# Kernel tuning notes

Measured on AMD Instinct MI355X. Metric: run time of the kernel, lower is better.

Reference implementation:

```python
import jax, jax.numpy as jnp
import numpy as np

N = 65536      # number of nodes being updated
EMBED = 1024   # embed_size
G = 256        # g_size (per-head dim)
MLP = 256      # mlp_size
H = 4          # n_head


def setup_inputs() -> dict:
    key = jax.random.key(0)
    ks = jax.random.split(key, 8)
    s_in = 1.0 / np.sqrt(EMBED)
    s_g = 1.0 / np.sqrt(G)
    s_m = 1.0 / np.sqrt(MLP)
    s_hg = 1.0 / np.sqrt(H * G)
    return {
        "q": jax.random.normal(ks[0], (N, EMBED), jnp.float32),
        "rep": jax.random.normal(ks[1], (N, EMBED), jnp.float32),
        "Wq": jax.random.normal(ks[2], (EMBED, H * G), jnp.float32) * s_in,
        "Wk": jax.random.normal(ks[3], (EMBED, H * G), jnp.float32) * s_in,
        "Wv": jax.random.normal(ks[4], (EMBED, H * G), jnp.float32) * s_in,
        "W1": jax.random.normal(ks[5], (H, G, MLP), jnp.float32) * s_g,
        "b1": jnp.zeros((H, MLP), jnp.float32),
        "W2": jax.random.normal(ks[6], (H, MLP, G), jnp.float32) * s_m,
        "b2": jnp.zeros((H, G), jnp.float32),
        "Ws": jax.random.normal(ks[7], (H * G, EMBED), jnp.float32) * s_hg,
    }


def reference(q, rep, Wq, Wk, Wv, W1, b1, W2, b2, Ws):
    # Per-head Q/K/V projections: [N, E] -> [N, H, G]
    n = q.shape[0]
    Qh = (q @ Wq).reshape(n, H, G)
    Kh = (rep @ Wk).reshape(n, H, G)
    Vh = (rep @ Wv).reshape(n, H, G)
    # Elementwise scaled attention gate (Q, K are per-node vectors -> 2D attn)
    gate = jax.nn.sigmoid(Qh * Kh * (1.0 / np.sqrt(G)))
    z = gate * Vh  # [N, H, G]
    # Per-head MLP (num_mlp = 1 block): G -> MLP -> G with ReLU
    h1 = jax.nn.relu(jnp.einsum('nhg,hgm->nhm', z, W1) + b1)
    z2 = jnp.einsum('nhm,hmg->nhg', h1, W2) + b2
    update_gate = z2.reshape(n, H * G)
    # update_attn_scale (no bias) + fused residual: h = Q - K + proj(gate)
    h = q - rep + update_gate @ Ws
    return h
```

## Files before the change

kernel.cpp:

```cpp
#include <hip/hip_runtime.h>
#include <hip/hip_bf16.h>


typedef __attribute__((ext_vector_type(8))) short bf16x8;
typedef __attribute__((ext_vector_type(4))) float f32x4;
typedef __attribute__((ext_vector_type(4))) short short4v;

#define AS1 __attribute__((address_space(1)))
#define AS3 __attribute__((address_space(3)))

static __device__ __forceinline__ short f2b(float x) {
  __hip_bfloat16 h = __float2bfloat16(x);
  return __builtin_bit_cast(short, h);
}
static __device__ __forceinline__ float b2f(short s) {
  unsigned u = ((unsigned)(unsigned short)s) << 16;
  return __builtin_bit_cast(float, u);
}

__global__ void cvt_bf16_2(const float* __restrict__ q, const float* __restrict__ rep,
                           short* __restrict__ qb, short* __restrict__ rb, long n) {
  const float* __restrict__ in = blockIdx.z ? rep : q;
  short* __restrict__ out = blockIdx.z ? rb : qb;
  long i = ((long)blockIdx.x * blockDim.x + threadIdx.x) * 4;
  const long stride = (long)gridDim.x * blockDim.x * 4;
  for (; i < n; i += stride) {
    float4 v = *(const float4*)(in + i);
    short4v o = { f2b(v.x), f2b(v.y), f2b(v.z), f2b(v.w) };
    *(short4v*)(out + i) = o;
  }
}

__global__ void prep_weights(
    const float* __restrict__ Wq, const float* __restrict__ Wk, const float* __restrict__ Wv,
    const float* __restrict__ W1, const float* __restrict__ W2, const float* __restrict__ Ws,
    short* __restrict__ wqt, short* __restrict__ wkt, short* __restrict__ wvt,
    short* __restrict__ w1t, short* __restrict__ w2t, short* __restrict__ wst)
{
  const int job = blockIdx.z;
  const float* src; short* dst; int R, C;
  if (job < 3)       { src = (job==0)?Wq:((job==1)?Wk:Wv); dst = (job==0)?wqt:((job==1)?wkt:wvt); R = 1024; C = 1024; }
  else if (job == 3) { src = Ws; dst = wst; R = 1024; C = 1024; }
  else if (job < 8)  { int h = job-4; src = W1 + h*65536; dst = w1t + h*65536; R = 256; C = 256; }
  else               { int h = job-8; src = W2 + h*65536; dst = w2t + h*65536; R = 256; C = 256; }
  const int c0 = blockIdx.x * 32, r0 = blockIdx.y * 32;
  if (c0 >= C || r0 >= R) return;
  __shared__ float t[32][33];
  for (int i = threadIdx.y; i < 32; i += 8)
    t[i][threadIdx.x] = src[(long)(r0 + i) * C + c0 + threadIdx.x];
  __syncthreads();
  for (int i = threadIdx.y; i < 32; i += 8)
    dst[(long)(c0 + i) * R + r0 + threadIdx.x] = f2b(t[threadIdx.x][i]);
}

template <int KDIM, int LDA, int LDB, bool RELU, bool BIAS, bool RESID, bool SWZ>
__global__ __launch_bounds__(512, 2) void gemm_bf16(
    const short* __restrict__ A, long zsa,
    const short* __restrict__ Bt, long zsb,
    void* __restrict__ outv, long ldc, long zsc,
    const float* __restrict__ bias, long zsbias,
    const short* __restrict__ qres, const short* __restrict__ rres)
{
  __shared__ __align__(16) short lA[4 * 8192];
  __shared__ __align__(16) short lB[4 * 8192];
  const int lane = threadIdx.x & 63, wave = threadIdx.x >> 6;
  const int wm = wave >> 2, wn = wave & 3;
  int bx = blockIdx.x, by = blockIdx.y;
  if (SWZ) {
    const int nbx = gridDim.x;
    const int flat = by * nbx + bx;
    const int chunk = (int)(gridDim.x * gridDim.y) >> 3;
    const int fid = (flat & 7) * chunk + (flat >> 3);
    bx = fid % nbx; by = fid / nbx;
  }
  const long bm = (long)by * 256;
  const int  bn = bx * 256;
  const int  zi = blockIdx.z;

  const short* Ab = A + (long)zi * zsa + bm * LDA;
  const short* Bb = Bt + (long)zi * zsb + (long)bn * LDB;
  constexpr int NS = KDIM / 32;
  const int g0 = lane >> 4;
  const int arow = wm * 128 + (lane & 15);
  const int bcol = wn * 64 + (lane & 15);

  const char* aP = (const char*)lA + arow * 64 + (((g0 ^ (arow >> 1)) & 3) << 4);
  const char* bP = (const char*)lB + bcol * 64 + (((g0 ^ (bcol >> 1)) & 3) << 4);

  const int rw = lane >> 2;
  const int gg = (lane & 3) ^ ((rw >> 1) & 3);
  const short* Asrc = Ab + (wave * 16 + rw) * LDA + (gg << 3);
  const short* Bsrc = Bb + (wave * 16 + rw) * LDB + (gg << 3);
  short* lAd = lA + wave * 16 * 32;
  short* lBd = lB + wave * 16 * 32;

  auto stA = [&](int slot, int s) {
    const int sc = s < NS ? s : NS - 1;
    const short* src = Asrc + sc * 32;
    short* d = lAd + slot * 8192;
    __builtin_amdgcn_global_load_lds((const AS1 void*)src,              (AS3 void*)d,        16, 0, 0);
    __builtin_amdgcn_global_load_lds((const AS1 void*)(src + 128*LDA),  (AS3 void*)(d+4096), 16, 0, 0);
  };
  auto stB = [&](int slot, int s) {
    const int sc = s < NS ? s : NS - 1;
    const short* src = Bsrc + sc * 32;
    short* d = lBd + slot * 8192;
    __builtin_amdgcn_global_load_lds((const AS1 void*)src,              (AS3 void*)d,        16, 0, 0);
    __builtin_amdgcn_global_load_lds((const AS1 void*)(src + 128*LDB),  (AS3 void*)(d+4096), 16, 0, 0);
  };

  stA(0, 0); stB(0, 0);
  stA(1, 1); stB(1, 1);
  stA(2, 2); stB(2, 2);
  asm volatile("s_waitcnt vmcnt(8)" ::: "memory");
  __builtin_amdgcn_s_barrier();

  f32x4 acc[8][4] = {};
  bf16x8 b[4];

#define PHASE(SLOT, MH, LOADB, STAGE_STMT, DOVM)                            \
  {                                                                         \
    if (LOADB) {                                                            \
      _Pragma("unroll")                                                     \
      for (int j = 0; j < 4; ++j)                                           \
        b[j] = *(const bf16x8*)(bP + (SLOT) * 16384 + j * 1024);            \
    }                                                                       \
    bf16x8 a[4];                                                            \
    _Pragma("unroll")                                                       \
    for (int i2 = 0; i2 < 4; ++i2)                                          \
      a[i2] = *(const bf16x8*)(aP + (SLOT) * 16384 + (MH) * 4096 + i2 * 1024); \
    STAGE_STMT;                                                             \
    if (DOVM) asm volatile("s_waitcnt vmcnt(8)" ::: "memory");              \
    asm volatile("" ::: "memory");                                          \
    __builtin_amdgcn_s_barrier();                                           \
    __builtin_amdgcn_s_setprio(1);                                          \
    _Pragma("unroll")                                                       \
    for (int i2 = 0; i2 < 4; ++i2)                                          \
      _Pragma("unroll")                                                     \
      for (int j = 0; j < 4; ++j)                                           \
        acc[(MH) * 4 + i2][j] = __builtin_amdgcn_mfma_f32_16x16x32_bf16(    \
            a[i2], b[j], acc[(MH) * 4 + i2][j], 0, 0, 0);                   \
    __builtin_amdgcn_s_setprio(0);                                          \
    asm volatile("" ::: "memory");                                          \
    __builtin_amdgcn_s_barrier();                                           \
  }

  for (int s = 0; s < NS; s += 4) {
    PHASE(0, 0, true,  stA(3, s + 3), false) PHASE(0, 1, false, stB(3, s + 3), true)
    PHASE(1, 0, true,  stA(0, s + 4), false) PHASE(1, 1, false, stB(0, s + 4), true)
    PHASE(2, 0, true,  stA(1, s + 5), false) PHASE(2, 1, false, stB(1, s + 5), true)
    PHASE(3, 0, true,  stA(2, s + 6), false) PHASE(3, 1, false, stB(2, s + 6), true)
  }
#undef PHASE

  #pragma unroll
  for (int i = 0; i < 8; ++i)
    #pragma unroll
    for (int j = 0; j < 4; ++j)
      #pragma unroll
      for (int r = 0; r < 4; ++r) {
        const int rl = wm * 128 + i * 16 + ((lane >> 4) << 2) + r;
        const int cl = wn * 64 + j * 16 + (lane & 15);
        float v = acc[i][j][r];
        if (BIAS) v += bias[(long)zi * zsbias + bn + cl];
        if (RELU) v = v > 0.0f ? v : 0.0f;
        const long row = bm + rl;
        const long gi = (long)zi * zsc + row * ldc + bn + cl;
        if (RESID) {
          ((float*)outv)[gi] = b2f(qres[gi]) - b2f(rres[gi]) + v;
        } else {
          ((short*)outv)[gi] = f2b(v);
        }
      }
}

__global__ __launch_bounds__(512, 2) void gemm_g23(
    const short* __restrict__ rb, const short* __restrict__ wkt,
    const short* __restrict__ wvt, const short* __restrict__ gh,
    short* __restrict__ zb)
{
  __shared__ __align__(16) short lA[4 * 8192];
  __shared__ __align__(16) short lK[4 * 4096];
  __shared__ __align__(16) short lV[4 * 4096];
  const int lane = threadIdx.x & 63, wave = threadIdx.x >> 6;
  const int wm = wave >> 2, wn = wave & 3;
  int bx = blockIdx.x, by = blockIdx.y;
  {
    const int flat = by * 8 + bx;
    const int chunk = (int)(gridDim.x * gridDim.y) >> 3;
    const int fid = (flat & 7) * chunk + (flat >> 3);
    bx = fid & 7; by = fid >> 3;
  }
  const long bm = (long)by * 256;
  const int  bn = bx * 128;

  const short* Ab = rb + bm * 1024;
  const short* Kb = wkt + (long)bn * 1024;
  const short* Vb = wvt + (long)bn * 1024;
  constexpr int NS = 32;
  const int g0 = lane >> 4;
  const int arow = wm * 128 + (lane & 15);
  const int bcol = wn * 32 + (lane & 15);

  const char* aP = (const char*)lA + arow * 64 + (((g0 ^ (arow >> 1)) & 3) << 4);
  const char* kP = (const char*)lK + bcol * 64 + (((g0 ^ (bcol >> 1)) & 3) << 4);
  const char* vP = (const char*)lV + bcol * 64 + (((g0 ^ (bcol >> 1)) & 3) << 4);

  const int rw = lane >> 2;
  const int gg = (lane & 3) ^ ((rw >> 1) & 3);
  const short* Asrc = Ab + (wave * 16 + rw) * 1024 + (gg << 3);
  const short* Ksrc = Kb + (wave * 16 + rw) * 1024 + (gg << 3);
  const short* Vsrc = Vb + (wave * 16 + rw) * 1024 + (gg << 3);
  short* lAd = lA + wave * 16 * 32;
  short* lKd = lK + wave * 16 * 32;
  short* lVd = lV + wave * 16 * 32;

  auto stA = [&](int slot, int s) {
    const int sc = s < NS ? s : NS - 1;
    const short* src = Asrc + sc * 32;
    short* d = lAd + slot * 8192;
    __builtin_amdgcn_global_load_lds((const AS1 void*)src,               (AS3 void*)d,        16, 0, 0);
    __builtin_amdgcn_global_load_lds((const AS1 void*)(src + 128*1024),  (AS3 void*)(d+4096), 16, 0, 0);
  };
  auto stKV = [&](int slot, int s) {
    const int sc = s < NS ? s : NS - 1;
    __builtin_amdgcn_global_load_lds((const AS1 void*)(Ksrc + sc * 32), (AS3 void*)(lKd + slot * 4096), 16, 0, 0);
    __builtin_amdgcn_global_load_lds((const AS1 void*)(Vsrc + sc * 32), (AS3 void*)(lVd + slot * 4096), 16, 0, 0);
  };

  stA(0, 0); stKV(0, 0);
  stA(1, 1); stKV(1, 1);
  stA(2, 2); stKV(2, 2);
  asm volatile("s_waitcnt vmcnt(8)" ::: "memory");
  __builtin_amdgcn_s_barrier();

  f32x4 ack[8][2] = {};
  f32x4 acv[8][2] = {};
  bf16x8 bk[2], bv[2];

#define PHASEG(SLOT, MH, LOADB, STAGE_STMT, DOVM)                           \
  {                                                                         \
    if (LOADB) {                                                            \
      _Pragma("unroll")                                                     \
      for (int j = 0; j < 2; ++j) {                                         \
        bk[j] = *(const bf16x8*)(kP + (SLOT) * 8192 + j * 1024);            \
        bv[j] = *(const bf16x8*)(vP + (SLOT) * 8192 + j * 1024);            \
      }                                                                     \
    }                                                                       \
    bf16x8 a[4];                                                            \
    _Pragma("unroll")                                                       \
    for (int i2 = 0; i2 < 4; ++i2)                                          \
      a[i2] = *(const bf16x8*)(aP + (SLOT) * 16384 + (MH) * 4096 + i2 * 1024); \
    STAGE_STMT;                                                             \
    if (DOVM) asm volatile("s_waitcnt vmcnt(8)" ::: "memory");              \
    asm volatile("" ::: "memory");                                          \
    __builtin_amdgcn_s_barrier();                                           \
    __builtin_amdgcn_s_setprio(1);                                          \
    _Pragma("unroll")                                                       \
    for (int i2 = 0; i2 < 4; ++i2)                                          \
      _Pragma("unroll")                                                     \
      for (int j = 0; j < 2; ++j) {                                         \
        ack[(MH) * 4 + i2][j] = __builtin_amdgcn_mfma_f32_16x16x32_bf16(    \
            a[i2], bk[j], ack[(MH) * 4 + i2][j], 0, 0, 0);                  \
        acv[(MH) * 4 + i2][j] = __builtin_amdgcn_mfma_f32_16x16x32_bf16(    \
            a[i2], bv[j], acv[(MH) * 4 + i2][j], 0, 0, 0);                  \
      }                                                                     \
    __builtin_amdgcn_s_setprio(0);                                          \
    asm volatile("" ::: "memory");                                          \
    __builtin_amdgcn_s_barrier();                                           \
  }

  for (int s = 0; s < NS; s += 4) {
    PHASEG(0, 0, true,  stA(3, s + 3), false) PHASEG(0, 1, false, stKV(3, s + 3), true)
    PHASEG(1, 0, true,  stA(0, s + 4), false) PHASEG(1, 1, false, stKV(0, s + 4), true)
    PHASEG(2, 0, true,  stA(1, s + 5), false) PHASEG(2, 1, false, stKV(1, s + 5), true)
    PHASEG(3, 0, true,  stA(2, s + 6), false) PHASEG(3, 1, false, stKV(2, s + 6), true)
  }
#undef PHASEG

  #pragma unroll
  for (int i = 0; i < 8; ++i)
    #pragma unroll
    for (int j = 0; j < 2; ++j)
      #pragma unroll
      for (int r = 0; r < 4; ++r) {
        const int rl = wm * 128 + i * 16 + ((lane >> 4) << 2) + r;
        const int cl = wn * 32 + j * 16 + (lane & 15);
        const long gi = (bm + rl) * 1024 + bn + cl;
        const float x = b2f(gh[gi]) * ack[i][j][r] * 0.0625f;
        const float gate = 1.0f / (1.0f + __expf(-x));
        zb[gi] = f2b(gate * acv[i][j][r]);
      }
}

__global__ __launch_bounds__(512) void gemm_mlp(
    const short* __restrict__ zb, const short* __restrict__ w1t,
    const short* __restrict__ w2t, const float* __restrict__ b1,
    const float* __restrict__ b2, short* __restrict__ ug)
{
  __shared__ __align__(16) char smem[163840];
  short* lA = (short*)smem;
  short* lB = (short*)(smem + 65536);
  short* stash = (short*)smem;
  short* w2b = (short*)(smem + 131072);

  const int lane = threadIdx.x & 63, wave = threadIdx.x >> 6;
  const int wm = wave >> 2, wn = wave & 3;
  const long bm = (long)blockIdx.y * 256;
  const int head = blockIdx.z;

  const int g0 = lane >> 4;
  const int arow = wm * 128 + (lane & 15);
  const int bcol = wn * 64 + (lane & 15);
  const int rw = lane >> 2;
  const int gg = (lane & 3) ^ ((rw >> 1) & 3);

  {
    const short* Ab = zb + bm * 1024 + head * 256;
    const short* Bb = w1t + head * 65536;
    const char* aP = (const char*)lA + arow * 64 + (((g0 ^ (arow >> 1)) & 3) << 4);
    const char* bP = (const char*)lB + bcol * 64 + (((g0 ^ (bcol >> 1)) & 3) << 4);
    const short* Asrc = Ab + (wave * 16 + rw) * 1024 + (gg << 3);
    const short* Bsrc = Bb + (wave * 16 + rw) * 256 + (gg << 3);
    short* lAd = lA + wave * 16 * 32;
    short* lBd = lB + wave * 16 * 32;

    auto stA = [&](int slot, int s) {
      const int sc = s < 8 ? s : 7;
      const short* src = Asrc + sc * 32;
      short* d = lAd + slot * 8192;
      __builtin_amdgcn_global_load_lds((const AS1 void*)src,              (AS3 void*)d,        16, 0, 0);
      __builtin_amdgcn_global_load_lds((const AS1 void*)(src + 128*1024), (AS3 void*)(d+4096), 16, 0, 0);
    };
    auto stB = [&](int slot, int s) {
      const int sc = s < 8 ? s : 7;
      const short* src = Bsrc + sc * 32;
      short* d = lBd + slot * 8192;
      __builtin_amdgcn_global_load_lds((const AS1 void*)src,              (AS3 void*)d,        16, 0, 0);
      __builtin_amdgcn_global_load_lds((const AS1 void*)(src + 128*256),  (AS3 void*)(d+4096), 16, 0, 0);
    };

    stA(0, 0); stB(0, 0);
    stA(1, 1); stB(1, 1);
    stA(2, 2); stB(2, 2);
    asm volatile("s_waitcnt vmcnt(8)" ::: "memory");
    __builtin_amdgcn_s_barrier();

    f32x4 acc[8][4] = {};
    bf16x8 b[4];

#define PHASE1(SLOT, MH, LOADB, STAGE_STMT, DOVM)                           \
    {                                                                       \
      if (LOADB) {                                                          \
        _Pragma("unroll")                                                   \
        for (int j = 0; j < 4; ++j)                                         \
          b[j] = *(const bf16x8*)(bP + (SLOT) * 16384 + j * 1024);          \
      }                                                                     \
      bf16x8 a[4];                                                          \
      _Pragma("unroll")                                                     \
      for (int i2 = 0; i2 < 4; ++i2)                                        \
        a[i2] = *(const bf16x8*)(aP + (SLOT) * 16384 + (MH) * 4096 + i2 * 1024); \
      STAGE_STMT;                                                           \
      if (DOVM) asm volatile("s_waitcnt vmcnt(8)" ::: "memory");            \
      asm volatile("" ::: "memory");                                        \
      __builtin_amdgcn_s_barrier();                                         \
      __builtin_amdgcn_s_setprio(1);                                        \
      _Pragma("unroll")                                                     \
      for (int i2 = 0; i2 < 4; ++i2)                                        \
        _Pragma("unroll")                                                   \
        for (int j = 0; j < 4; ++j)                                         \
          acc[(MH) * 4 + i2][j] = __builtin_amdgcn_mfma_f32_16x16x32_bf16(  \
              a[i2], b[j], acc[(MH) * 4 + i2][j], 0, 0, 0);                 \
      __builtin_amdgcn_s_setprio(0);                                        \
      asm volatile("" ::: "memory");                                        \
      __builtin_amdgcn_s_barrier();                                         \
    }

    for (int s = 0; s < 8; s += 4) {
      PHASE1(0, 0, true,  stA(3, s + 3), false) PHASE1(0, 1, false, stB(3, s + 3), true)
      PHASE1(1, 0, true,  stA(0, s + 4), false) PHASE1(1, 1, false, stB(0, s + 4), true)
      PHASE1(2, 0, true,  stA(1, s + 5), false) PHASE1(2, 1, false, stB(1, s + 5), true)
      PHASE1(3, 0, true,  stA(2, s + 6), false) PHASE1(3, 1, false, stB(2, s + 6), true)
    }
#undef PHASE1

    __syncthreads();
    #pragma unroll
    for (int i = 0; i < 8; ++i)
      #pragma unroll
      for (int j = 0; j < 4; ++j)
        #pragma unroll
        for (int r = 0; r < 4; ++r) {
          const int rl = wm * 128 + i * 16 + ((lane >> 4) << 2) + r;
          const int cl = wn * 64 + j * 16 + (lane & 15);
          float v = acc[i][j][r] + b1[head * 256 + cl];
          v = v > 0.0f ? v : 0.0f;
          stash[rl * 256 + ((((cl >> 3) ^ rl) & 31) << 3) + (cl & 7)] = f2b(v);
        }
    __syncthreads();
  }

  {
    const short* Wb = w2t + head * 65536;
    const short* Bsrc2 = Wb + (wave * 16 + rw) * 256 + (gg << 3);
    short* lBd2 = w2b + wave * 16 * 32;
    const char* b2P = (const char*)w2b + bcol * 64 + (((g0 ^ (bcol >> 1)) & 3) << 4);

    auto stW = [&](int slot, int s) {
      const int sc = s < 8 ? s : 7;
      const short* src = Bsrc2 + sc * 32;
      short* d = lBd2 + slot * 8192;
      __builtin_amdgcn_global_load_lds((const AS1 void*)src,             (AS3 void*)d,        16, 0, 0);
      __builtin_amdgcn_global_load_lds((const AS1 void*)(src + 128*256), (AS3 void*)(d+4096), 16, 0, 0);
    };

    stW(0, 0);
    asm volatile("s_waitcnt vmcnt(0)" ::: "memory");
    __builtin_amdgcn_s_barrier();

    f32x4 acc2[8][4] = {};
    bf16x8 br[4];

    for (int s = 0; s < 8; ++s) {
      const int sl = s & 1;
      const int ks = s * 4 + g0;

#define PHASE2(MH, LOADB, STAGE_STMT, DOVM)                                 \
      {                                                                     \
        if (LOADB) {                                                        \
          _Pragma("unroll")                                                 \
          for (int j = 0; j < 4; ++j)                                       \
            br[j] = *(const bf16x8*)(b2P + sl * 16384 + j * 1024);          \
        }                                                                   \
        bf16x8 a[4];                                                        \
        _Pragma("unroll")                                                   \
        for (int i2 = 0; i2 < 4; ++i2) {                                    \
          const int row = arow + (MH) * 64 + i2 * 16;                       \
          a[i2] = *(const bf16x8*)(stash + row * 256 + (((ks ^ row) & 31) << 3)); \
        }                                                                   \
        STAGE_STMT;                                                         \
        if (DOVM) asm volatile("s_waitcnt vmcnt(0)" ::: "memory");          \
        asm volatile("" ::: "memory");                                      \
        __builtin_amdgcn_s_barrier();                                       \
        __builtin_amdgcn_s_setprio(1);                                      \
        _Pragma("unroll")                                                   \
        for (int i2 = 0; i2 < 4; ++i2)                                      \
          _Pragma("unroll")                                                 \
          for (int j = 0; j < 4; ++j)                                       \
            acc2[(MH) * 4 + i2][j] = __builtin_amdgcn_mfma_f32_16x16x32_bf16( \
                a[i2], br[j], acc2[(MH) * 4 + i2][j], 0, 0, 0);             \
        __builtin_amdgcn_s_setprio(0);                                      \
        asm volatile("" ::: "memory");                                      \
        __builtin_amdgcn_s_barrier();                                       \
      }

      PHASE2(0, true,  stW(sl ^ 1, s + 1), false)
      PHASE2(1, false, {}, true)
#undef PHASE2
    }

    #pragma unroll
    for (int i = 0; i < 8; ++i)
      #pragma unroll
      for (int j = 0; j < 4; ++j)
        #pragma unroll
        for (int r = 0; r < 4; ++r) {
          const int rl = wm * 128 + i * 16 + ((lane >> 4) << 2) + r;
          const int cl = wn * 64 + j * 16 + (lane & 15);
          const float v = acc2[i][j][r] + b2[head * 256 + cl];
          ug[(bm + rl) * 1024 + head * 256 + cl] = f2b(v);
        }
  }
}

extern "C" void kernel_launch(void* const* d_in, const int* in_sizes, int n_in,
                              void* d_out, int out_size, void* d_ws, size_t ws_size,
                              hipStream_t stream) {
  const float* q   = (const float*)d_in[0];
  const float* rep = (const float*)d_in[1];
  const float* Wq  = (const float*)d_in[2];
  const float* Wk  = (const float*)d_in[3];
  const float* Wv  = (const float*)d_in[4];
  const float* W1  = (const float*)d_in[5];
  const float* b1  = (const float*)d_in[6];
  const float* W2  = (const float*)d_in[7];
  const float* b2  = (const float*)d_in[8];
  const float* Ws  = (const float*)d_in[9];
  float* out = (float*)d_out;

  const long NE = 67108864L;
  char* ws = (char*)d_ws;
  short* qb  = (short*)(ws);
  short* rb  = (short*)(ws + NE * 2);
  short* gh  = (short*)(ws + NE * 4);
  short* zb  = (short*)(ws + NE * 6);
  short* ugb = gh;
  char*  wp  = ws + NE * 8;
  short* wqt = (short*)(wp);
  short* wkt = (short*)(wp + 2097152);
  short* wvt = (short*)(wp + 4194304);
  short* wst = (short*)(wp + 6291456);
  short* w1t = (short*)(wp + 8388608);
  short* w2t = (short*)(wp + 8912896);

  cvt_bf16_2<<<dim3(2048, 1, 2), 256, 0, stream>>>(q, rep, qb, rb, NE);
  prep_weights<<<dim3(32, 32, 12), dim3(32, 8), 0, stream>>>(
      Wq, Wk, Wv, W1, W2, Ws, wqt, wkt, wvt, w1t, w2t, wst);

  gemm_bf16<1024, 1024, 1024, false, false, false, true><<<dim3(4, 256), 512, 0, stream>>>(
      qb, 0, wqt, 0, gh, 1024, 0, nullptr, 0, nullptr, nullptr);
  gemm_g23<<<dim3(8, 256), 512, 0, stream>>>(rb, wkt, wvt, gh, zb);
  gemm_mlp<<<dim3(1, 256, 4), 512, 0, stream>>>(zb, w1t, w2t, b1, b2, ugb);
  gemm_bf16<1024, 1024, 1024, false, false, true, true><<<dim3(4, 256), 512, 0, stream>>>(
      ugb, 0, wst, 0, out, 1024, 0, nullptr, 0, qb, rb);
}
```

Before: 1.002 ms.

## Fuse Q projection into gated K/V GEMM kernel, dropping Q intermediate

The separate Q-projection GEMM and its bf16 intermediate buffer are removed. Q is now computed in the same kernel as K and V, so the sigmoid gate uses the Q accumulator directly instead of reading a stored Q tile. To fit the extra operand tiles in LDS, the pipeline is cut from four stages to two, and each stage waits for all outstanding loads (vmcnt(0)). This saves one kernel launch plus the write and reread of a 128MB intermediate. In exchange it adds accumulator register pressure and gives less latency hiding.

```diff
diff --git a/kernel.cpp b/kernel.cpp
--- a/kernel.cpp
+++ b/kernel.cpp
@@ -174,14 +174,19 @@
       }
 }
 
-__global__ __launch_bounds__(512, 2) void gemm_g23(
-    const short* __restrict__ rb, const short* __restrict__ wkt,
-    const short* __restrict__ wvt, const short* __restrict__ gh,
+__global__ __launch_bounds__(512, 2) void gemm_g123(
+    const short* __restrict__ qb,
+    const short* __restrict__ rb,
+    const short* __restrict__ wqt,
+    const short* __restrict__ wkt,
+    const short* __restrict__ wvt,
     short* __restrict__ zb)
 {
-  __shared__ __align__(16) short lA[4 * 8192];
-  __shared__ __align__(16) short lK[4 * 4096];
-  __shared__ __align__(16) short lV[4 * 4096];
+  __shared__ __align__(16) short lAq[2 * 8192];
+  __shared__ __align__(16) short lAr[2 * 8192];
+  __shared__ __align__(16) short lQ[2 * 4096];
+  __shared__ __align__(16) short lK[2 * 4096];
+  __shared__ __align__(16) short lV[2 * 4096];
   const int lane = threadIdx.x & 63, wave = threadIdx.x >> 6;
   const int wm = wave >> 2, wn = wave & 3;
   int bx = blockIdx.x, by = blockIdx.y;
@@ -194,7 +199,9 @@
   const long bm = (long)by * 256;
   const int  bn = bx * 128;
 
-  const short* Ab = rb + bm * 1024;
+  const short* Aqb = qb + bm * 1024;
+  const short* Arb = rb + bm * 1024;
+  const short* Qb = wqt + (long)bn * 1024;
   const short* Kb = wkt + (long)bn * 1024;
   const short* Vb = wvt + (long)bn * 1024;
   constexpr int NS = 32;
@@ -202,81 +209,95 @@
   const int arow = wm * 128 + (lane & 15);
   const int bcol = wn * 32 + (lane & 15);
 
-  const char* aP = (const char*)lA + arow * 64 + (((g0 ^ (arow >> 1)) & 3) << 4);
+  const char* aPq = (const char*)lAq + arow * 64 + (((g0 ^ (arow >> 1)) & 3) << 4);
+  const char* aPr = (const char*)lAr + arow * 64 + (((g0 ^ (arow >> 1)) & 3) << 4);
+  const char* qP = (const char*)lQ + bcol * 64 + (((g0 ^ (bcol >> 1)) & 3) << 4);
   const char* kP = (const char*)lK + bcol * 64 + (((g0 ^ (bcol >> 1)) & 3) << 4);
   const char* vP = (const char*)lV + bcol * 64 + (((g0 ^ (bcol >> 1)) & 3) << 4);
 
   const int rw = lane >> 2;
   const int gg = (lane & 3) ^ ((rw >> 1) & 3);
-  const short* Asrc = Ab + (wave * 16 + rw) * 1024 + (gg << 3);
+  const short* Aqsrc = Aqb + (wave * 16 + rw) * 1024 + (gg << 3);
+  const short* Arsrc = Arb + (wave * 16 + rw) * 1024 + (gg << 3);
+  const short* Qsrc = Qb + (wave * 16 + rw) * 1024 + (gg << 3);
   const short* Ksrc = Kb + (wave * 16 + rw) * 1024 + (gg << 3);
   const short* Vsrc = Vb + (wave * 16 + rw) * 1024 + (gg << 3);
-  short* lAd = lA + wave * 16 * 32;
+  short* lAqd = lAq + wave * 16 * 32;
+  short* lArd = lAr + wave * 16 * 32;
+  short* lQd = lQ + wave * 16 * 32;
   short* lKd = lK + wave * 16 * 32;
   short* lVd = lV + wave * 16 * 32;
 
-  auto stA = [&](int slot, int s) {
+  auto stAll = [&](int slot, int s) {
     const int sc = s < NS ? s : NS - 1;
-    const short* src = Asrc + sc * 32;
-    short* d = lAd + slot * 8192;
-    __builtin_amdgcn_global_load_lds((const AS1 void*)src,               (AS3 void*)d,        16, 0, 0);
-    __builtin_amdgcn_global_load_lds((const AS1 void*)(src + 128*1024),  (AS3 void*)(d+4096), 16, 0, 0);
-  };
-  auto stKV = [&](int slot, int s) {
-    const int sc = s < NS ? s : NS - 1;
+    const short* sq = Aqsrc + sc * 32;
+    const short* sr = Arsrc + sc * 32;
+    short* dq = lAqd + slot * 8192;
+    short* dr = lArd + slot * 8192;
+    __builtin_amdgcn_global_load_lds((const AS1 void*)sq,               (AS3 void*)dq,        16, 0, 0);
+    __builtin_amdgcn_global_load_lds((const AS1 void*)(sq + 128*1024),  (AS3 void*)(dq+4096), 16, 0, 0);
+    __builtin_amdgcn_global_load_lds((const AS1 void*)sr,               (AS3 void*)dr,        16, 0, 0);
+    __builtin_amdgcn_global_load_lds((const AS1 void*)(sr + 128*1024),  (AS3 void*)(dr+4096), 16, 0, 0);
+    __builtin_amdgcn_global_load_lds((const AS1 void*)(Qsrc + sc * 32), (AS3 void*)(lQd + slot * 4096), 16, 0, 0);
     __builtin_amdgcn_global_load_lds((const AS1 void*)(Ksrc + sc * 32), (AS3 void*)(lKd + slot * 4096), 16, 0, 0);
     __builtin_amdgcn_global_load_lds((const AS1 void*)(Vsrc + sc * 32), (AS3 void*)(lVd + slot * 4096), 16, 0, 0);
   };
 
-  stA(0, 0); stKV(0, 0);
-  stA(1, 1); stKV(1, 1);
-  stA(2, 2); stKV(2, 2);
-  asm volatile("s_waitcnt vmcnt(8)" ::: "memory");
+  stAll(0, 0);
+  asm volatile("s_waitcnt vmcnt(0)" ::: "memory");
   __builtin_amdgcn_s_barrier();
 
+  f32x4 acq[8][2] = {};
   f32x4 ack[8][2] = {};
   f32x4 acv[8][2] = {};
-  bf16x8 bk[2], bv[2];
-
-#define PHASEG(SLOT, MH, LOADB, STAGE_STMT, DOVM)                           \
+  bf16x8 bq[2], bk[2], bv[2];
+
+#define PHASEQ(SLOT, MH, LOADB, STAGE_STMT, DOVM)                           \
   {                                                                         \
     if (LOADB) {                                                            \
       _Pragma("unroll")                                                     \
       for (int j = 0; j < 2; ++j) {                                         \
+        bq[j] = *(const bf16x8*)(qP + (SLOT) * 8192 + j * 1024);            \
         bk[j] = *(const bf16x8*)(kP + (SLOT) * 8192 + j * 1024);            \
         bv[j] = *(const bf16x8*)(vP + (SLOT) * 8192 + j * 1024);            \
       }                                                                     \
     }                                                                       \
-    bf16x8 a[4];                                                            \
-    _Pragma("unroll")                                                       \
-    for (int i2 = 0; i2 < 4; ++i2)                                          \
-      a[i2] = *(const bf16x8*)(aP + (SLOT) * 16384 + (MH) * 4096 + i2 * 1024); \
     STAGE_STMT;                                                             \
-    if (DOVM) asm volatile("s_waitcnt vmcnt(8)" ::: "memory");              \
+    if (DOVM) asm volatile("s_waitcnt vmcnt(0)" ::: "memory");              \
     asm volatile("" ::: "memory");                                          \
     __builtin_amdgcn_s_barrier();                                           \
     __builtin_amdgcn_s_setprio(1);                                          \
     _Pragma("unroll")                                                       \
-    for (int i2 = 0; i2 < 4; ++i2)                                          \
+    for (int i2 = 0; i2 < 4; ++i2) {                                        \
+      const bf16x8 aq = *(const bf16x8*)(aPq + (SLOT) * 16384 + (MH) * 4096 + i2 * 1024); \
+      _Pragma("unroll")                                                     \
+      for (int j = 0; j < 2; ++j)                                           \
+        acq[(MH) * 4 + i2][j] = __builtin_amdgcn_mfma_f32_16x16x32_bf16(    \
+            aq, bq[j], acq[(MH) * 4 + i2][j], 0, 0, 0);                     \
+    }                                                                       \
+    _Pragma("unroll")                                                       \
+    for (int i2 = 0; i2 < 4; ++i2) {                                        \
+      const bf16x8 ar = *(const bf16x8*)(aPr + (SLOT) * 16384 + (MH) * 4096 + i2 * 1024); \
       _Pragma("unroll")                                                     \
       for (int j = 0; j < 2; ++j) {                                         \
         ack[(MH) * 4 + i2][j] = __builtin_amdgcn_mfma_f32_16x16x32_bf16(    \
-            a[i2], bk[j], ack[(MH) * 4 + i2][j], 0, 0, 0);                  \
+            ar, bk[j], ack[(MH) * 4 + i2][j], 0, 0, 0);                     \
         acv[(MH) * 4 + i2][j] = __builtin_amdgcn_mfma_f32_16x16x32_bf16(    \
-            a[i2], bv[j], acv[(MH) * 4 + i2][j], 0, 0, 0);                  \
+            ar, bv[j], acv[(MH) * 4 + i2][j], 0, 0, 0);                     \
       }                                                                     \
+    }                                                                       \
     __builtin_amdgcn_s_setprio(0);                                          \
     asm volatile("" ::: "memory");                                          \
     __builtin_amdgcn_s_barrier();                                           \
   }
 
-  for (int s = 0; s < NS; s += 4) {
-    PHASEG(0, 0, true,  stA(3, s + 3), false) PHASEG(0, 1, false, stKV(3, s + 3), true)
-    PHASEG(1, 0, true,  stA(0, s + 4), false) PHASEG(1, 1, false, stKV(0, s + 4), true)
-    PHASEG(2, 0, true,  stA(1, s + 5), false) PHASEG(2, 1, false, stKV(1, s + 5), true)
-    PHASEG(3, 0, true,  stA(2, s + 6), false) PHASEG(3, 1, false, stKV(2, s + 6), true)
-  }
-#undef PHASEG
+  for (int s = 0; s < NS; s += 2) {
+    PHASEQ(0, 0, true,  stAll(1, s + 1), false)
+    PHASEQ(0, 1, false, {}, true)
+    PHASEQ(1, 0, true,  stAll(0, s + 2), false)
+    PHASEQ(1, 1, false, {}, true)
+  }
+#undef PHASEQ
 
   #pragma unroll
   for (int i = 0; i < 8; ++i)
@@ -287,7 +308,7 @@
         const int rl = wm * 128 + i * 16 + ((lane >> 4) << 2) + r;
         const int cl = wn * 32 + j * 16 + (lane & 15);
         const long gi = (bm + rl) * 1024 + bn + cl;
-        const float x = b2f(gh[gi]) * ack[i][j][r] * 0.0625f;
+        const float x = acq[i][j][r] * ack[i][j][r] * 0.0625f;
         const float gate = 1.0f / (1.0f + __expf(-x));
         zb[gi] = f2b(gate * acv[i][j][r]);
       }
@@ -492,9 +513,8 @@
   char* ws = (char*)d_ws;
   short* qb  = (short*)(ws);
   short* rb  = (short*)(ws + NE * 2);
-  short* gh  = (short*)(ws + NE * 4);
+  short* ugb = (short*)(ws + NE * 4);
   short* zb  = (short*)(ws + NE * 6);
-  short* ugb = gh;
   char*  wp  = ws + NE * 8;
   short* wqt = (short*)(wp);
   short* wkt = (short*)(wp + 2097152);
@@ -507,9 +527,7 @@
   prep_weights<<<dim3(32, 32, 12), dim3(32, 8), 0, stream>>>(
       Wq, Wk, Wv, W1, W2, Ws, wqt, wkt, wvt, w1t, w2t, wst);
 
-  gemm_bf16<1024, 1024, 1024, false, false, false, true><<<dim3(4, 256), 512, 0, stream>>>(
-      qb, 0, wqt, 0, gh, 1024, 0, nullptr, 0, nullptr, nullptr);
-  gemm_g23<<<dim3(8, 256), 512, 0, stream>>>(rb, wkt, wvt, gh, zb);
+  gemm_g123<<<dim3(8, 256), 512, 0, stream>>>(qb, rb, wqt, wkt, wvt, zb);
   gemm_mlp<<<dim3(1, 256, 4), 512, 0, stream>>>(zb, w1t, w2t, b1, b2, ugb);
   gemm_bf16<1024, 1024, 1024, false, false, true, true><<<dim3(4, 256), 512, 0, stream>>>(
       ugb, 0, wst, 0, out, 1024, 0, nullptr, 0, qb, rb);
```

Measured after the change: 1.073 ms. +7.0%, slower.

## Use 4-wave blocks with 128x128 warp tiles in the dense projection GEMMs

Applied to the files above, without the earlier changes.

Replaces the 8-wave, 512-thread GEMM with a 256-thread, 4-wave version. Each wave now computes a 128x128 sub-tile (8x8 MFMA accumulators) of the same 256x256 block tile. The K slice is consumed in one phase per stage with a single barrier pair, instead of two half-phases. This raises MFMA work per LDS fragment read and halves barrier count, but uses far more accumulator registers (256 VGPRs of acc) and limits occupancy to one block per CU.

```diff
diff --git a/kernel.cpp b/kernel.cpp
--- a/kernel.cpp
+++ b/kernel.cpp
@@ -53,20 +53,18 @@
     dst[(long)(c0 + i) * R + r0 + threadIdx.x] = f2b(t[threadIdx.x][i]);
 }
 
-template <int KDIM, int LDA, int LDB, bool RELU, bool BIAS, bool RESID, bool SWZ>
-__global__ __launch_bounds__(512, 2) void gemm_bf16(
-    const short* __restrict__ A, long zsa,
-    const short* __restrict__ Bt, long zsb,
-    void* __restrict__ outv, long ldc, long zsc,
-    const float* __restrict__ bias, long zsbias,
+template <int KDIM, bool RESID>
+__global__ __launch_bounds__(256, 1) void gemm_rb(
+    const short* __restrict__ A, const short* __restrict__ Bt,
+    void* __restrict__ outv,
     const short* __restrict__ qres, const short* __restrict__ rres)
 {
   __shared__ __align__(16) short lA[4 * 8192];
   __shared__ __align__(16) short lB[4 * 8192];
   const int lane = threadIdx.x & 63, wave = threadIdx.x >> 6;
-  const int wm = wave >> 2, wn = wave & 3;
+  const int wm = wave >> 1, wn = wave & 1;
   int bx = blockIdx.x, by = blockIdx.y;
-  if (SWZ) {
+  {
     const int nbx = gridDim.x;
     const int flat = by * nbx + bx;
     const int chunk = (int)(gridDim.x * gridDim.y) >> 3;
@@ -75,22 +73,21 @@
   }
   const long bm = (long)by * 256;
   const int  bn = bx * 256;
-  const int  zi = blockIdx.z;
-
-  const short* Ab = A + (long)zi * zsa + bm * LDA;
-  const short* Bb = Bt + (long)zi * zsb + (long)bn * LDB;
+
+  const short* Ab = A + bm * 1024;
+  const short* Bb = Bt + (long)bn * 1024;
   constexpr int NS = KDIM / 32;
   const int g0 = lane >> 4;
   const int arow = wm * 128 + (lane & 15);
-  const int bcol = wn * 64 + (lane & 15);
+  const int bcol = wn * 128 + (lane & 15);
 
   const char* aP = (const char*)lA + arow * 64 + (((g0 ^ (arow >> 1)) & 3) << 4);
   const char* bP = (const char*)lB + bcol * 64 + (((g0 ^ (bcol >> 1)) & 3) << 4);
 
   const int rw = lane >> 2;
   const int gg = (lane & 3) ^ ((rw >> 1) & 3);
-  const short* Asrc = Ab + (wave * 16 + rw) * LDA + (gg << 3);
-  const short* Bsrc = Bb + (wave * 16 + rw) * LDB + (gg << 3);
+  const short* Asrc = Ab + (wave * 16 + rw) * 1024 + (gg << 3);
+  const short* Bsrc = Bb + (wave * 16 + rw) * 1024 + (gg << 3);
   short* lAd = lA + wave * 16 * 32;
   short* lBd = lB + wave * 16 * 32;
 
@@ -98,74 +95,72 @@
     const int sc = s < NS ? s : NS - 1;
     const short* src = Asrc + sc * 32;
     short* d = lAd + slot * 8192;
-    __builtin_amdgcn_global_load_lds((const AS1 void*)src,              (AS3 void*)d,        16, 0, 0);
-    __builtin_amdgcn_global_load_lds((const AS1 void*)(src + 128*LDA),  (AS3 void*)(d+4096), 16, 0, 0);
+    #pragma unroll
+    for (int j = 0; j < 4; ++j)
+      __builtin_amdgcn_global_load_lds((const AS1 void*)(src + (long)j * 64 * 1024),
+                                       (AS3 void*)(d + j * 64 * 32), 16, 0, 0);
   };
   auto stB = [&](int slot, int s) {
     const int sc = s < NS ? s : NS - 1;
     const short* src = Bsrc + sc * 32;
     short* d = lBd + slot * 8192;
-    __builtin_amdgcn_global_load_lds((const AS1 void*)src,              (AS3 void*)d,        16, 0, 0);
-    __builtin_amdgcn_global_load_lds((const AS1 void*)(src + 128*LDB),  (AS3 void*)(d+4096), 16, 0, 0);
+    #pragma unroll
+    for (int j = 0; j < 4; ++j)
+      __builtin_amdgcn_global_load_lds((const AS1 void*)(src + (long)j * 64 * 1024),
+                                       (AS3 void*)(d + j * 64 * 32), 16, 0, 0);
   };
 
   stA(0, 0); stB(0, 0);
   stA(1, 1); stB(1, 1);
   stA(2, 2); stB(2, 2);
-  asm volatile("s_waitcnt vmcnt(8)" ::: "memory");
+  asm volatile("s_waitcnt vmcnt(16)" ::: "memory");
   __builtin_amdgcn_s_barrier();
 
-  f32x4 acc[8][4] = {};
-  bf16x8 b[4];
-
-#define PHASE(SLOT, MH, LOADB, STAGE_STMT, DOVM)                            \
+  f32x4 acc[8][8] = {};
+
+#define SLICE(SLOT, STSLOT, SNEXT)                                          \
   {                                                                         \
-    if (LOADB) {                                                            \
-      _Pragma("unroll")                                                     \
-      for (int j = 0; j < 4; ++j)                                           \
-        b[j] = *(const bf16x8*)(bP + (SLOT) * 16384 + j * 1024);            \
-    }                                                                       \
-    bf16x8 a[4];                                                            \
+    bf16x8 a[8], b[8];                                                      \
     _Pragma("unroll")                                                       \
-    for (int i2 = 0; i2 < 4; ++i2)                                          \
-      a[i2] = *(const bf16x8*)(aP + (SLOT) * 16384 + (MH) * 4096 + i2 * 1024); \
-    STAGE_STMT;                                                             \
-    if (DOVM) asm volatile("s_waitcnt vmcnt(8)" ::: "memory");              \
+    for (int j = 0; j < 8; ++j)                                             \
+      b[j] = *(const bf16x8*)(bP + (SLOT) * 16384 + j * 1024);              \
+    _Pragma("unroll")                                                       \
+    for (int i = 0; i < 8; ++i)                                             \
+      a[i] = *(const bf16x8*)(aP + (SLOT) * 16384 + i * 1024);              \
+    stA(STSLOT, SNEXT); stB(STSLOT, SNEXT);                                 \
+    asm volatile("s_waitcnt vmcnt(16)" ::: "memory");                       \
     asm volatile("" ::: "memory");                                          \
     __builtin_amdgcn_s_barrier();                                           \
     __builtin_amdgcn_s_setprio(1);                                          \
     _Pragma("unroll")                                                       \
-    for (int i2 = 0; i2 < 4; ++i2)                                          \
+    for (int i = 0; i < 8; ++i)                                             \
       _Pragma("unroll")                                                     \
-      for (int j = 0; j < 4; ++j)                                           \
-        acc[(MH) * 4 + i2][j] = __builtin_amdgcn_mfma_f32_16x16x32_bf16(    \
-            a[i2], b[j], acc[(MH) * 4 + i2][j], 0, 0, 0);                   \
+      for (int j = 0; j < 8; ++j)                                           \
+        acc[i][j] = __builtin_amdgcn_mfma_f32_16x16x32_bf16(                \
+            a[i], b[j], acc[i][j], 0, 0, 0);                                \
     __builtin_amdgcn_s_setprio(0);                                          \
     asm volatile("" ::: "memory");                                          \
     __builtin_amdgcn_s_barrier();                                           \
   }
 
   for (int s = 0; s < NS; s += 4) {
-    PHASE(0, 0, true,  stA(3, s + 3), false) PHASE(0, 1, false, stB(3, s + 3), true)
-    PHASE(1, 0, true,  stA(0, s + 4), false) PHASE(1, 1, false, stB(0, s + 4), true)
-    PHASE(2, 0, true,  stA(1, s + 5), false) PHASE(2, 1, false, stB(1, s + 5), true)
-    PHASE(3, 0, true,  stA(2, s + 6), false) PHASE(3, 1, false, stB(2, s + 6), true)
-  }
-#undef PHASE
+    SLICE(0, 3, s + 3)
+    SLICE(1, 0, s + 4)
+    SLICE(2, 1, s + 5)
+    SLICE(3, 2, s + 6)
+  }
+#undef SLICE
 
   #pragma unroll
   for (int i = 0; i < 8; ++i)
     #pragma unroll
-    for (int j = 0; j < 4; ++j)
+    for (int j = 0; j < 8; ++j)
       #pragma unroll
       for (int r = 0; r < 4; ++r) {
         const int rl = wm * 128 + i * 16 + ((lane >> 4) << 2) + r;
-        const int cl = wn * 64 + j * 16 + (lane & 15);
-        float v = acc[i][j][r];
-        if (BIAS) v += bias[(long)zi * zsbias + bn + cl];
-        if (RELU) v = v > 0.0f ? v : 0.0f;
-        const long row = bm + rl;
-        const long gi = (long)zi * zsc + row * ldc + bn + cl;
+        const int cl = wn * 128 + j * 16 + (lane & 15);
+        const float v = acc[i][j][r];
+        const long gi = (bm + rl) * 1024 + bn + cl;
         if (RESID) {
           ((float*)outv)[gi] = b2f(qres[gi]) - b2f(rres[gi]) + v;
         } else {
@@ -507,10 +502,10 @@
   prep_weights<<<dim3(32, 32, 12), dim3(32, 8), 0, stream>>>(
       Wq, Wk, Wv, W1, W2, Ws, wqt, wkt, wvt, w1t, w2t, wst);
 
-  gemm_bf16<1024, 1024, 1024, false, false, false, true><<<dim3(4, 256), 512, 0, stream>>>(
-      qb, 0, wqt, 0, gh, 1024, 0, nullptr, 0, nullptr, nullptr);
+  gemm_rb<1024, false><<<dim3(4, 256), 256, 0, stream>>>(
+      qb, wqt, gh, nullptr, nullptr);
   gemm_g23<<<dim3(8, 256), 512, 0, stream>>>(rb, wkt, wvt, gh, zb);
   gemm_mlp<<<dim3(1, 256, 4), 512, 0, stream>>>(zb, w1t, w2t, b1, b2, ugb);
-  gemm_bf16<1024, 1024, 1024, false, false, true, true><<<dim3(4, 256), 512, 0, stream>>>(
-      ugb, 0, wst, 0, out, 1024, 0, nullptr, 0, qb, rb);
-}
+  gemm_rb<1024, true><<<dim3(4, 256), 256, 0, stream>>>(
+      ugb, wst, out, qb, rb);
+}
```

Result: slower. 1.493 ms (+48.9%).
